# Kernel optimization log

Measured on AMD Instinct MI355X. Metric: run time of the kernel, lower is better.

The kernel has to match this reference:

```python
import jax, jax.numpy as jnp
import numpy as np
import math

DIM = 4096
N_HEADS = 32
HEAD_DIM = DIM // N_HEADS  # 128


def setup_inputs() -> dict:
    key = jax.random.key(0)
    ks = jax.random.split(key, 10)
    B, S, C = 2, 1024, 2048
    x = jax.random.normal(ks[0], (B, S, DIM), dtype=jnp.float32)
    freqs_cis = jax.random.normal(ks[1], (S, HEAD_DIM // 2), dtype=jnp.float32)
    mask = jnp.zeros((1, 1, S, C), dtype=jnp.float32)
    input_idexes = jnp.arange(S, dtype=jnp.int64) if jax.config.jax_enable_x64 else jnp.arange(S, dtype=jnp.int32)
    cache_k = jax.random.normal(ks[2], (B, C, N_HEADS, HEAD_DIM), dtype=jnp.float32) * 0.1
    cache_v = jax.random.normal(ks[3], (B, C, N_HEADS, HEAD_DIM), dtype=jnp.float32) * 0.1
    # Linear weights in torch layout [out_features, in_features], y = x @ W.T
    wq = jax.random.normal(ks[4], (DIM, DIM), dtype=jnp.float32) * 0.02
    wk = jax.random.normal(ks[5], (DIM, DIM), dtype=jnp.float32) * 0.02
    wv = jax.random.normal(ks[6], (DIM, DIM), dtype=jnp.float32) * 0.02
    wo = jax.random.normal(ks[7], (DIM, DIM), dtype=jnp.float32) * 0.02
    return {"x": x, "freqs_cis": freqs_cis, "mask": mask, "input_idexes": input_idexes,
            "cache_k": cache_k, "cache_v": cache_v, "wq": wq, "wk": wk, "wv": wv, "wo": wo}


def reference(x, freqs_cis, mask, input_idexes, cache_k, cache_v, wq, wk, wv, wo):
    B, S, D = x.shape
    H, hd = N_HEADS, HEAD_DIM
    # projections (torch Linear: x @ W.T)
    xq = jnp.einsum('bsd,ed->bse', x, wq).reshape(B, S, H, hd)
    # xk/xv are computed in the original forward but never used (cache-only attention)
    xk = jnp.einsum('bsd,ed->bse', x, wk).reshape(B, S, H, hd)  # noqa: F841
    xv = jnp.einsum('bsd,ed->bse', x, wv).reshape(B, S, H, hd)  # noqa: F841
    q = xq.transpose(0, 2, 1, 3)                 # [B,H,S,hd]
    keys = cache_k.transpose(0, 2, 1, 3)         # [B,H,C,hd]
    values = cache_v.transpose(0, 2, 1, 3)       # [B,H,C,hd]
    scores = jnp.einsum('bhse,bhce->bhsc', q, keys) / math.sqrt(hd)
    scores = scores + mask
    attn = jax.nn.softmax(scores.astype(jnp.float32), axis=-1).astype(q.dtype)
    out = jnp.einsum('bhsc,bhce->bhse', attn, values)  # [B,H,S,hd]
    out = out.transpose(0, 2, 1, 3).reshape(B, S, H * hd)
    return jnp.einsum('bse,de->bsd', out, wo)
```

## Files before the change

kernel.cpp:

```cpp
#include <hip/hip_runtime.h>
#include <hip/hip_bf16.h>
#include <stdint.h>


#define DIM   4096
#define NH    32
#define HD    128
#define BB    2
#define SS    1024
#define CC    2048

typedef __bf16 bf16x8 __attribute__((ext_vector_type(8)));
typedef float  f32x4  __attribute__((ext_vector_type(4)));

__device__ __forceinline__ unsigned short f2bf(float f) {
  union { __hip_bfloat16 h; unsigned short u; } cv;
  cv.h = __float2bfloat16(f);
  return cv.u;
}

__device__ __forceinline__ void gl_lds16(const void* g, void* l) {
  __builtin_amdgcn_global_load_lds(
      (__attribute__((address_space(1))) void*)(uintptr_t)(g),
      (__attribute__((address_space(3))) void*)(l), 16, 0, 0);
}

__global__ void conv_f32_bf16(const float* __restrict__ in, unsigned short* __restrict__ out, int n4) {
  int i = blockIdx.x * blockDim.x + threadIdx.x;
  int stride = gridDim.x * blockDim.x;
  for (; i < n4; i += stride) {
    float4 v = reinterpret_cast<const float4*>(in)[i];
    ushort4 o;
    o.x = f2bf(v.x); o.y = f2bf(v.y); o.z = f2bf(v.z); o.w = f2bf(v.w);
    reinterpret_cast<ushort4*>(out)[i] = o;
  }
}

__global__ void conv_k(const float* __restrict__ in, unsigned short* __restrict__ out) {
  const int total4 = BB * NH * CC * HD / 4;
  int i = blockIdx.x * blockDim.x + threadIdx.x;
  int stride = gridDim.x * blockDim.x;
  for (; i < total4; i += stride) {
    size_t o = (size_t)i * 4;
    int d   = (int)(o & (HD - 1));
    size_t r = o >> 7;
    int c   = (int)(r & (CC - 1));
    int bh  = (int)(r >> 11);
    int hh = bh & (NH - 1), bb = bh >> 5;
    float4 v = *reinterpret_cast<const float4*>(in + ((size_t)(bb * CC + c) * NH + hh) * HD + d);
    ushort4 u; u.x = f2bf(v.x); u.y = f2bf(v.y); u.z = f2bf(v.z); u.w = f2bf(v.w);
    *reinterpret_cast<ushort4*>(out + o) = u;
  }
}

__global__ void conv_v_t(const float* __restrict__ in, unsigned short* __restrict__ out) {
  __shared__ float tile[32][33];
  const int c0 = blockIdx.x * 32, d0 = blockIdx.y * 32;
  const int bh = blockIdx.z;
  const int hh = bh & (NH - 1), bb = bh >> 5;
  const int tx = threadIdx.x, ty = threadIdx.y;
#pragma unroll
  for (int i = 0; i < 4; ++i) {
    int c = c0 + ty + i * 8;
    tile[ty + i * 8][tx] = in[((size_t)(bb * CC + c) * NH + hh) * HD + d0 + tx];
  }
  __syncthreads();
#pragma unroll
  for (int i = 0; i < 4; ++i) {
    int d = d0 + ty + i * 8;
    out[((size_t)bh * HD + d) * CC + c0 + tx] = f2bf(tile[tx][ty + i * 8]);
  }
}

template <int OUT_BF16>
__global__ __launch_bounds__(256, 2) void gemm_bt(
    const unsigned short* __restrict__ A,
    const unsigned short* __restrict__ Bw,
    void* __restrict__ Cout,
    int M, int N, int K, float scale)
{
  __shared__ __align__(16) unsigned short As[128 * 32];
  __shared__ __align__(16) unsigned short Bs[128 * 32];
  const int t = threadIdx.x;
  const int w = t >> 6, lane = t & 63;
  const int wr = w >> 1, wc = w & 1;
  const int bm0 = blockIdx.y * 128, bn0 = blockIdx.x * 128;

  const unsigned short* aSrc = A  + (size_t)(bm0 + (t >> 2)) * K + (t & 3) * 8;
  const unsigned short* bSrc = Bw + (size_t)(bn0 + (t >> 2)) * K + (t & 3) * 8;
  char* aDst = (char*)As + w * 1024;
  char* bDst = (char*)Bs + w * 1024;
  const size_t half = (size_t)64 * K;

  f32x4 acc[4][4];
#pragma unroll
  for (int m = 0; m < 4; ++m)
#pragma unroll
    for (int n = 0; n < 4; ++n) acc[m][n] = (f32x4){0.f, 0.f, 0.f, 0.f};

  for (int k0 = 0; k0 < K; k0 += 32) {
    gl_lds16(aSrc,        aDst);
    gl_lds16(aSrc + half, aDst + 4096);
    gl_lds16(bSrc,        bDst);
    gl_lds16(bSrc + half, bDst + 4096);
    aSrc += 32; bSrc += 32;
    __syncthreads();

    bf16x8 af[4], bf[4];
#pragma unroll
    for (int m = 0; m < 4; ++m)
      af[m] = *(const bf16x8*)&As[(wr * 64 + m * 16 + (lane & 15)) * 32 + (lane >> 4) * 8];
#pragma unroll
    for (int n = 0; n < 4; ++n)
      bf[n] = *(const bf16x8*)&Bs[(wc * 64 + n * 16 + (lane & 15)) * 32 + (lane >> 4) * 8];
#pragma unroll
    for (int m = 0; m < 4; ++m)
#pragma unroll
      for (int n = 0; n < 4; ++n)
        acc[m][n] = __builtin_amdgcn_mfma_f32_16x16x32_bf16(af[m], bf[n], acc[m][n], 0, 0, 0);
    __syncthreads();
  }

  const int r0 = (lane >> 4) * 4, cl = lane & 15;
#pragma unroll
  for (int m = 0; m < 4; ++m) {
#pragma unroll
    for (int n = 0; n < 4; ++n) {
      int row = bm0 + wr * 64 + m * 16 + r0;
      int col = bn0 + wc * 64 + n * 16 + cl;
#pragma unroll
      for (int r = 0; r < 4; ++r) {
        float v = acc[m][n][r] * scale;
        if (OUT_BF16) ((unsigned short*)Cout)[(size_t)(row + r) * N + col] = f2bf(v);
        else          ((float*)Cout)[(size_t)(row + r) * N + col] = v;
      }
    }
  }
}

__global__ __launch_bounds__(256, 2) void attn_fwd(
    const unsigned short* __restrict__ Qb,
    const unsigned short* __restrict__ Kb,
    const unsigned short* __restrict__ Vtb,
    const float* __restrict__ mask,
    unsigned short* __restrict__ Ob)
{
  __shared__ __align__(16) unsigned short Ks[2][64 * 128];
  __shared__ __align__(16) unsigned short Vs[2][64 * 128];
  __shared__ __align__(16) unsigned short Ps[4][32 * 64];

  const int t = threadIdx.x, w = t >> 6, lane = t & 63;
  const int bid = blockIdx.x;
  const int qt = bid & 7, bh = bid >> 3;
  const int hh = bh & (NH - 1), bb = bh >> 5;
  const int q0 = qt * 128;
  const int l15 = lane & 15, g = lane >> 4;
  const int rb4 = g * 4;

  bf16x8 qf[2][4];
#pragma unroll
  for (int rf = 0; rf < 2; ++rf) {
    const unsigned short* qp = Qb + ((size_t)(bb * SS + q0 + w * 32 + rf * 16 + l15)) * DIM
                               + hh * HD + g * 8;
#pragma unroll
    for (int kk = 0; kk < 4; ++kk)
      qf[rf][kk] = *(const bf16x8*)(qp + kk * 32);
  }

  const unsigned short* kSrc = Kb + ((size_t)bh * CC + (t >> 4)) * HD
                               + (((t & 15) ^ ((t >> 4) & 7)) * 8);
  const unsigned short* vSrc = Vtb + ((size_t)bh * HD + (t >> 3)) * CC
                               + (((t & 7) ^ ((t >> 3) & 7)) * 8);

  f32x4 acc_o[2][8];
#pragma unroll
  for (int rf = 0; rf < 2; ++rf)
#pragma unroll
    for (int i = 0; i < 8; ++i) acc_o[rf][i] = (f32x4){0.f, 0.f, 0.f, 0.f};
  float m_run[2][4], l_run[2][4];
#pragma unroll
  for (int rf = 0; rf < 2; ++rf)
#pragma unroll
    for (int r = 0; r < 4; ++r) { m_run[rf][r] = -1e30f; l_run[rf][r] = 0.f; }

  const int swz = (lane & 7) << 3;
  const float LOG2E = 1.4426950408889634f;

  {
    char* kd = (char*)Ks[0] + w * 1024;
    char* vd = (char*)Vs[0] + w * 1024;
#pragma unroll
    for (int i = 0; i < 4; ++i) {
      gl_lds16(kSrc + (size_t)(i * 16) * HD, kd + i * 4096);
      gl_lds16(vSrc + (size_t)i * 32 * CC,   vd + i * 4096);
    }
  }
  __syncthreads();

  int cur = 0;
  for (int c0 = 0; c0 < CC; c0 += 64) {
    float mk[2][4][4];
#pragma unroll
    for (int rf = 0; rf < 2; ++rf)
#pragma unroll
      for (int nf = 0; nf < 4; ++nf)
#pragma unroll
        for (int r = 0; r < 4; ++r)
          mk[rf][nf][r] = mask[(size_t)(q0 + w * 32 + rf * 16 + rb4 + r) * CC
                               + c0 + nf * 16 + l15];
    __builtin_amdgcn_sched_barrier(0);

    if (c0 + 64 < CC) {
      char* kd = (char*)Ks[cur ^ 1] + w * 1024;
      char* vd = (char*)Vs[cur ^ 1] + w * 1024;
#pragma unroll
      for (int i = 0; i < 4; ++i) {
        gl_lds16(kSrc + (size_t)(c0 + 64 + i * 16) * HD, kd + i * 4096);
        gl_lds16(vSrc + (size_t)i * 32 * CC + c0 + 64,   vd + i * 4096);
      }
    }
    __builtin_amdgcn_sched_barrier(0);

    f32x4 sc[2][4];
#pragma unroll
    for (int rf = 0; rf < 2; ++rf)
#pragma unroll
      for (int nf = 0; nf < 4; ++nf) sc[rf][nf] = (f32x4){0.f, 0.f, 0.f, 0.f};
    __builtin_amdgcn_s_setprio(1);
#pragma unroll
    for (int kk = 0; kk < 4; ++kk) {
#pragma unroll
      for (int nf = 0; nf < 4; ++nf) {
        bf16x8 kf = *(const bf16x8*)&Ks[cur][((nf * 16 + l15) * 128 + kk * 32 + g * 8) ^ swz];
        sc[0][nf] = __builtin_amdgcn_mfma_f32_16x16x32_bf16(qf[0][kk], kf, sc[0][nf], 0, 0, 0);
        sc[1][nf] = __builtin_amdgcn_mfma_f32_16x16x32_bf16(qf[1][kk], kf, sc[1][nf], 0, 0, 0);
      }
    }
    __builtin_amdgcn_s_setprio(0);

#pragma unroll
    for (int rf = 0; rf < 2; ++rf) {
#pragma unroll
      for (int nf = 0; nf < 4; ++nf)
#pragma unroll
        for (int r = 0; r < 4; ++r)
          sc[rf][nf][r] = fmaf(mk[rf][nf][r], LOG2E, sc[rf][nf][r]);

      int ok = 1;
      float pm[4];
#pragma unroll
      for (int r = 0; r < 4; ++r) {
        pm[r] = fmaxf(fmaxf(sc[rf][0][r], sc[rf][1][r]), fmaxf(sc[rf][2][r], sc[rf][3][r]));
        ok = ok && (pm[r] <= m_run[rf][r] + 8.0f);
      }
      if (!__all(ok)) {
#pragma unroll
        for (int r = 0; r < 4; ++r) {
          float mx = pm[r];
#pragma unroll
          for (int d = 1; d < 16; d <<= 1)
            mx = fmaxf(mx, __shfl_xor(mx, d));
          float mn = fmaxf(m_run[rf][r], mx);
          float corr = __builtin_amdgcn_exp2f(m_run[rf][r] - mn);
          m_run[rf][r] = mn;
          l_run[rf][r] *= corr;
#pragma unroll
          for (int nd = 0; nd < 8; ++nd) acc_o[rf][nd][r] *= corr;
        }
      }

#pragma unroll
      for (int r = 0; r < 4; ++r) {
        int rw = rf * 16 + rb4 + r;
        int rsw = (rw & 7) << 3;
#pragma unroll
        for (int nf = 0; nf < 4; ++nf) {
          float p = __builtin_amdgcn_exp2f(sc[rf][nf][r] - m_run[rf][r]);
          l_run[rf][r] += p;
          Ps[w][rw * 64 + ((nf * 16 + l15) ^ rsw)] = f2bf(p);
        }
      }
    }

    __builtin_amdgcn_s_setprio(1);
#pragma unroll
    for (int kk = 0; kk < 2; ++kk) {
      bf16x8 pf0 = *(const bf16x8*)&Ps[w][((0 * 16 + l15) * 64 + kk * 32 + g * 8) ^ swz];
      bf16x8 pf1 = *(const bf16x8*)&Ps[w][((1 * 16 + l15) * 64 + kk * 32 + g * 8) ^ swz];
#pragma unroll
      for (int nd = 0; nd < 8; ++nd) {
        bf16x8 vf = *(const bf16x8*)&Vs[cur][((nd * 16 + l15) * 64 + kk * 32 + g * 8) ^ swz];
        acc_o[0][nd] = __builtin_amdgcn_mfma_f32_16x16x32_bf16(pf0, vf, acc_o[0][nd], 0, 0, 0);
        acc_o[1][nd] = __builtin_amdgcn_mfma_f32_16x16x32_bf16(pf1, vf, acc_o[1][nd], 0, 0, 0);
      }
    }
    __builtin_amdgcn_s_setprio(0);
    __syncthreads();
    cur ^= 1;
  }

#pragma unroll
  for (int rf = 0; rf < 2; ++rf) {
#pragma unroll
    for (int r = 0; r < 4; ++r)
#pragma unroll
      for (int d = 1; d < 16; d <<= 1)
        l_run[rf][r] += __shfl_xor(l_run[rf][r], d);

#pragma unroll
    for (int nd = 0; nd < 8; ++nd)
#pragma unroll
      for (int r = 0; r < 4; ++r) {
        float v = acc_o[rf][nd][r] / l_run[rf][r];
        int row = q0 + w * 32 + rf * 16 + rb4 + r;
        Ob[(size_t)(bb * SS + row) * DIM + hh * HD + nd * 16 + l15] = f2bf(v);
      }
  }
}

extern "C" void kernel_launch(void* const* d_in, const int* in_sizes, int n_in,
                              void* d_out, int out_size, void* d_ws, size_t ws_size,
                              hipStream_t stream) {
  const float* x       = (const float*)d_in[0];
  const float* mask    = (const float*)d_in[2];
  const float* cache_k = (const float*)d_in[4];
  const float* cache_v = (const float*)d_in[5];
  const float* wq      = (const float*)d_in[6];
  const float* wo      = (const float*)d_in[9];
  float* out = (float*)d_out;

  char* ws = (char*)d_ws;
  unsigned short* Wbf  = (unsigned short*)(ws);
  unsigned short* xbf  = (unsigned short*)(ws + 33554432);
  unsigned short* qbf  = (unsigned short*)(ws + 33554432 + 16777216);
  unsigned short* kbf  = (unsigned short*)(ws + 33554432 + 2 * 16777216);
  unsigned short* vtbf = (unsigned short*)(ws + 2 * 33554432 + 2 * 16777216);

  conv_f32_bf16<<<2048, 256, 0, stream>>>(x,  xbf, BB * SS * DIM / 4);
  conv_f32_bf16<<<2048, 256, 0, stream>>>(wq, Wbf, DIM * DIM / 4);
  dim3 gg(DIM / 128, (BB * SS) / 128);
  gemm_bt<1><<<gg, 256, 0, stream>>>(xbf, Wbf, qbf, BB * SS, DIM, DIM, 0.12751744682f);
  conv_k<<<2048, 256, 0, stream>>>(cache_k, kbf);
  conv_v_t<<<dim3(CC / 32, HD / 32, BB * NH), dim3(32, 8, 1), 0, stream>>>(cache_v, vtbf);
  attn_fwd<<<BB * NH * 8, 256, 0, stream>>>(qbf, kbf, vtbf, mask, xbf);
  conv_f32_bf16<<<2048, 256, 0, stream>>>(wo, Wbf, DIM * DIM / 4);
  gemm_bt<0><<<gg, 256, 0, stream>>>(xbf, Wbf, out, BB * SS, DIM, DIM, 1.0f);
}
```

Baseline: 395.9 us.

## Skip all-zero mask tiles via precomputed flags and remap block order

Adds a small kernel that scans the mask in 128x64 tiles and records whether each tile holds any nonzero value, storing the flags in the output buffer as scratch. The attention kernel reads these flags and skips the mask loads and adds for zero tiles, which removes a large stream of fp32 mask reads. It also remaps block indices in the GEMM and attention kernels to group blocks that share data for better L2 reuse. The flag scan is a real per-call pass over the mask, so results stay correct for any mask, at the cost of one extra launch.

```diff
diff --git a/kernel.cpp b/kernel.cpp
--- a/kernel.cpp
+++ b/kernel.cpp
@@ -72,6 +72,25 @@
   }
 }
 
+__global__ void mask_flags(const float* __restrict__ mask, int* __restrict__ flags) {
+  __shared__ int s[4];
+  const int qt = blockIdx.x >> 5, ct = blockIdx.x & 31;
+  const int t = threadIdx.x, w = t >> 6;
+  const float4* m4 = (const float4*)mask;
+  int nz = 0;
+#pragma unroll
+  for (int i = 0; i < 8; ++i) {
+    int idx = i * 256 + t;
+    int row = idx >> 4, c4 = idx & 15;
+    float4 v = m4[(size_t)(qt * 128 + row) * (CC / 4) + ct * 16 + c4];
+    nz |= (v.x != 0.f) | (v.y != 0.f) | (v.z != 0.f) | (v.w != 0.f);
+  }
+  int wa = (int)__any(nz);
+  if ((t & 63) == 0) s[w] = wa;
+  __syncthreads();
+  if (t == 0) flags[qt * 32 + ct] = s[0] | s[1] | s[2] | s[3];
+}
+
 template <int OUT_BF16>
 __global__ __launch_bounds__(256, 2) void gemm_bt(
     const unsigned short* __restrict__ A,
@@ -84,7 +103,10 @@
   const int t = threadIdx.x;
   const int w = t >> 6, lane = t & 63;
   const int wr = w >> 1, wc = w & 1;
-  const int bm0 = blockIdx.y * 128, bn0 = blockIdx.x * 128;
+  const int nwg  = gridDim.x * gridDim.y;
+  const int flat = blockIdx.y * gridDim.x + blockIdx.x;
+  const int swzb = (flat & 7) * (nwg >> 3) + (flat >> 3);
+  const int bm0 = (swzb / gridDim.x) * 128, bn0 = (swzb % gridDim.x) * 128;
 
   const unsigned short* aSrc = A  + (size_t)(bm0 + (t >> 2)) * K + (t & 3) * 8;
   const unsigned short* bSrc = Bw + (size_t)(bn0 + (t >> 2)) * K + (t & 3) * 8;
@@ -143,6 +165,7 @@
     const unsigned short* __restrict__ Kb,
     const unsigned short* __restrict__ Vtb,
     const float* __restrict__ mask,
+    const int* __restrict__ Mf,
     unsigned short* __restrict__ Ob)
 {
   __shared__ __align__(16) unsigned short Ks[2][64 * 128];
@@ -150,8 +173,8 @@
   __shared__ __align__(16) unsigned short Ps[4][32 * 64];
 
   const int t = threadIdx.x, w = t >> 6, lane = t & 63;
-  const int bid = blockIdx.x;
-  const int qt = bid & 7, bh = bid >> 3;
+  const int lg = (blockIdx.x & 7) * 64 + (blockIdx.x >> 3);
+  const int qt = lg & 7, bh = lg >> 3;
   const int hh = bh & (NH - 1), bb = bh >> 5;
   const int q0 = qt * 128;
   const int l15 = lane & 15, g = lane >> 4;
@@ -186,6 +209,7 @@
   const int swz = (lane & 7) << 3;
   const float LOG2E = 1.4426950408889634f;
 
+  int mflag = Mf[qt * 32];
   {
     char* kd = (char*)Ks[0] + w * 1024;
     char* vd = (char*)Vs[0] + w * 1024;
@@ -199,16 +223,21 @@
 
   int cur = 0;
   for (int c0 = 0; c0 < CC; c0 += 64) {
+    const int ct = c0 >> 6;
+    int nextFlag = (ct < 31) ? Mf[qt * 32 + ct + 1] : 0;
+
     float mk[2][4][4];
-#pragma unroll
-    for (int rf = 0; rf < 2; ++rf)
-#pragma unroll
-      for (int nf = 0; nf < 4; ++nf)
-#pragma unroll
-        for (int r = 0; r < 4; ++r)
-          mk[rf][nf][r] = mask[(size_t)(q0 + w * 32 + rf * 16 + rb4 + r) * CC
-                               + c0 + nf * 16 + l15];
-    __builtin_amdgcn_sched_barrier(0);
+    if (mflag) {
+#pragma unroll
+      for (int rf = 0; rf < 2; ++rf)
+#pragma unroll
+        for (int nf = 0; nf < 4; ++nf)
+#pragma unroll
+          for (int r = 0; r < 4; ++r)
+            mk[rf][nf][r] = mask[(size_t)(q0 + w * 32 + rf * 16 + rb4 + r) * CC
+                                 + c0 + nf * 16 + l15];
+      __builtin_amdgcn_sched_barrier(0);
+    }
 
     if (c0 + 64 < CC) {
       char* kd = (char*)Ks[cur ^ 1] + w * 1024;
@@ -238,14 +267,18 @@
     }
     __builtin_amdgcn_s_setprio(0);
 
+    if (mflag) {
+#pragma unroll
+      for (int rf = 0; rf < 2; ++rf)
+#pragma unroll
+        for (int nf = 0; nf < 4; ++nf)
+#pragma unroll
+          for (int r = 0; r < 4; ++r)
+            sc[rf][nf][r] = fmaf(mk[rf][nf][r], LOG2E, sc[rf][nf][r]);
+    }
+
 #pragma unroll
     for (int rf = 0; rf < 2; ++rf) {
-#pragma unroll
-      for (int nf = 0; nf < 4; ++nf)
-#pragma unroll
-        for (int r = 0; r < 4; ++r)
-          sc[rf][nf][r] = fmaf(mk[rf][nf][r], LOG2E, sc[rf][nf][r]);
-
       int ok = 1;
       float pm[4];
 #pragma unroll
@@ -297,6 +330,7 @@
     __builtin_amdgcn_s_setprio(0);
     __syncthreads();
     cur ^= 1;
+    mflag = nextFlag;
   }
 
 #pragma unroll
@@ -335,6 +369,7 @@
   unsigned short* qbf  = (unsigned short*)(ws + 33554432 + 16777216);
   unsigned short* kbf  = (unsigned short*)(ws + 33554432 + 2 * 16777216);
   unsigned short* vtbf = (unsigned short*)(ws + 2 * 33554432 + 2 * 16777216);
+  int* mflags = (int*)d_out;
 
   conv_f32_bf16<<<2048, 256, 0, stream>>>(x,  xbf, BB * SS * DIM / 4);
   conv_f32_bf16<<<2048, 256, 0, stream>>>(wq, Wbf, DIM * DIM / 4);
@@ -342,7 +377,8 @@
   gemm_bt<1><<<gg, 256, 0, stream>>>(xbf, Wbf, qbf, BB * SS, DIM, DIM, 0.12751744682f);
   conv_k<<<2048, 256, 0, stream>>>(cache_k, kbf);
   conv_v_t<<<dim3(CC / 32, HD / 32, BB * NH), dim3(32, 8, 1), 0, stream>>>(cache_v, vtbf);
-  attn_fwd<<<BB * NH * 8, 256, 0, stream>>>(qbf, kbf, vtbf, mask, xbf);
+  mask_flags<<<256, 256, 0, stream>>>(mask, mflags);
+  attn_fwd<<<BB * NH * 8, 256, 0, stream>>>(qbf, kbf, vtbf, mask, mflags, xbf);
   conv_f32_bf16<<<2048, 256, 0, stream>>>(wo, Wbf, DIM * DIM / 4);
   gemm_bt<0><<<gg, 256, 0, stream>>>(xbf, Wbf, out, BB * SS, DIM, DIM, 1.0f);
 }
```

Result: faster. 371.6 us (-6.1%).
